# Kernel tuning notes

Hardware: AMD Instinct MI355X
Metric: run time of the kernel (lower is better)

## Reference

```python
import jax, jax.numpy as jnp
import numpy as np
from jax import lax

B, C, H, W = 8, 1, 256, 256
BIG = float(H + W)  # larger than any possible in-image distance


def _dist_1d_along_h(feat):
    # feat: bool (B,H,W). Exact 1D distance along axis 1 to nearest True pixel.
    def step(d, f):
        d = jnp.where(f, 0.0, d + 1.0)
        return d, d

    init = jnp.full((feat.shape[0], feat.shape[2]), BIG, dtype=jnp.float32)
    ft = jnp.moveaxis(feat, 1, 0)  # (H,B,W)
    _, fwd = lax.scan(step, init, ft)
    _, bwd = lax.scan(step, init, ft[::-1])
    g = jnp.minimum(fwd, bwd[::-1])  # (H,B,W)
    return jnp.moveaxis(g, 0, 1)  # (B,H,W)


def _edt(feat):
    # Exact 2D Euclidean distance transform to nearest True pixel.
    # Decomposition: D2(i,j) = min_{j'} ( g(i,j')^2 + (j-j')^2 ),
    # where g is the exact 1D vertical distance within each column.
    g = jnp.minimum(_dist_1d_along_h(feat), BIG)
    g2 = g * g  # (B,H,W')
    j = jnp.arange(feat.shape[2], dtype=jnp.float32)
    offs = (j[:, None] - j[None, :]) ** 2  # (W, W')
    d2 = jnp.min(g2[:, :, None, :] + offs[None, None, :, :], axis=-1)  # (B,H,W)
    return jnp.sqrt(d2)


def _level_set(targets):
    # Faithful port of compute_level_set_function.
    m = targets[:, 0] != 0  # (B,H,W) foreground
    # scipy.distance_transform_edt(mask): distance of nonzero pixels to nearest zero -> features = background
    dist_inside = _edt(~m)
    # distance_transform_edt(1-mask): features = foreground
    dist_outside = _edt(m)
    phi = dist_outside - dist_inside
    denom = jnp.max(jnp.abs(phi), axis=(1, 2), keepdims=True) + 1e-8
    phi = phi / denom
    has_fg = jnp.any(m, axis=(1, 2), keepdims=True)
    phi = jnp.where(has_fg, phi, 0.0)  # empty-mask short-circuit -> zeros
    return phi[:, None].astype(jnp.float32)  # (B,1,H,W)


def setup_inputs() -> dict:
    key = jax.random.key(0)
    k1, k2 = jax.random.split(key)
    predictions = jax.random.normal(k1, (B, C, H, W), dtype=jnp.float32)
    targets = jax.random.randint(k2, (B, C, H, W), 0, 2, dtype=jnp.int32)
    return {"predictions": predictions, "targets": targets}


def reference(predictions, targets):
    probs = jax.nn.sigmoid(predictions)
    phi_G = _level_set(targets)
    return jnp.mean(phi_G * probs)
```

## Files before the change

### kernel.cpp

```cpp
#include <hip/hip_runtime.h>
#include <math.h>

#define BB 8
#define HH 256
#define WW 256
#define NPIX (BB*HH*WW)
#define NROWS (BB*HH)


__global__ void colscan(const int* __restrict__ tgt,
                        float2* __restrict__ g2,
                        int* __restrict__ hasfg8) {
    __shared__ int hiF[8][32], loF[8][32], hiB[8][32], loB[8][32];
    __shared__ int wany[4];
    int tx = threadIdx.x;
    int c = tx & 31, s = tx >> 5;
    int bw = blockIdx.x;
    int b = bw >> 3;
    int w = ((bw & 7) << 5) + c;
    const int* col = tgt + b * HH * WW + w;
    int base = s << 5;

    unsigned fgbits = 0;
    #pragma unroll
    for (int r = 0; r < 32; ++r)
        fgbits |= (col[(base + r) * WW] != 0 ? 1u : 0u) << r;
    unsigned bgbits = ~fgbits;

    hiF[s][c] = fgbits ? (base + 31 - __clz(fgbits)) : -1;
    loF[s][c] = fgbits ? (base + __ffs(fgbits) - 1) : -1;
    hiB[s][c] = bgbits ? (base + 31 - __clz(bgbits)) : -1;
    loB[s][c] = bgbits ? (base + __ffs(bgbits) - 1) : -1;
    unsigned long long bal = __ballot(fgbits != 0);
    if ((tx & 63) == 0) wany[tx >> 6] = (bal != 0ull);
    __syncthreads();

    int prevF = -100000, nextF = 100000, prevB = -100000, nextB = 100000;
    for (int t = 0; t < s; ++t) {
        int h = hiF[t][c]; if (h >= 0) prevF = h;
        int g = hiB[t][c]; if (g >= 0) prevB = g;
    }
    for (int t = 7; t > s; --t) {
        int l = loF[t][c]; if (l >= 0) nextF = l;
        int m = loB[t][c]; if (m >= 0) nextB = m;
    }

    float2* out = g2 + b * HH * WW + w;
    #pragma unroll
    for (int r = 0; r < 32; ++r) {
        int i = base + r;
        unsigned lowmask = 0xFFFFFFFFu >> (31 - r);

        unsigned mf = fgbits & lowmask;
        int pF = mf ? (base + 31 - __clz(mf)) : prevF;
        unsigned nf = fgbits >> r;
        int nF = nf ? (i + __ffs(nf) - 1) : nextF;
        int gFg = min(min(i - pF, nF - i), 512);

        unsigned mb = bgbits & lowmask;
        int pB = mb ? (base + 31 - __clz(mb)) : prevB;
        unsigned nb = bgbits >> r;
        int nB = nb ? (i + __ffs(nb) - 1) : nextB;
        int gBg = min(min(i - pB, nB - i), 512);

        float fa = (float)gBg;
        float fb = (float)gFg;
        float2 o; o.x = fa * fa; o.y = fb * fb;
        out[i * WW] = o;
    }

    if (tx == 0)
        hasfg8[bw] = wany[0] | wany[1] | wany[2] | wany[3];
}

__global__ void edt_fuse(const float2* __restrict__ g2,
                         const float* __restrict__ pred,
                         float* __restrict__ part_max,
                         double* __restrict__ part_sum) {
    __shared__ float sB[3 * WW];
    __shared__ float sF[3 * WW];
    __shared__ float wmax[4];
    __shared__ double wsum[4];
    int row = blockIdx.x;
    int j = threadIdx.x;

    float x = pred[row * WW + j];
    float2 v = g2[row * WW + j];
    sB[j] = 1e30f; sB[2 * WW + j] = 1e30f; sB[WW + j] = v.x;
    sF[j] = 1e30f; sF[2 * WW + j] = 1e30f; sF[WW + j] = v.y;
    bool isBg = (v.x == 0.0f);
    __syncthreads();

    const float* sp = isBg ? sF : sB;
    float m = isBg ? v.y : v.x;
    int idx = WW + j;
    for (int k = 1; k < WW; ++k) {
        float k2 = (float)(k * k);
        if (k2 >= m) break;
        m = fminf(m, sp[idx - k] + k2);
        m = fminf(m, sp[idx + k] + k2);
    }
    float dist = sqrtf(m);
    float phi = isBg ? dist : -dist;
    float prob = 1.0f / (1.0f + expf(-x));
    double sd = (double)(phi * prob);
    float mx = dist;

    #pragma unroll
    for (int off = 32; off; off >>= 1) {
        mx = fmaxf(mx, __shfl_down(mx, off));
        sd += __shfl_down(sd, off);
    }
    int wid = j >> 6;
    if ((j & 63) == 0) { wmax[wid] = mx; wsum[wid] = sd; }
    __syncthreads();
    if (j == 0) {
        part_max[row] = fmaxf(fmaxf(wmax[0], wmax[1]), fmaxf(wmax[2], wmax[3]));
        part_sum[row] = wsum[0] + wsum[1] + wsum[2] + wsum[3];
    }
}

__global__ void reduce_out(const float* __restrict__ part_max,
                           const double* __restrict__ part_sum,
                           const int* __restrict__ hasfg8,
                           float* __restrict__ out) {
    __shared__ float wmax[4];
    __shared__ double wsum[4];
    int t = threadIdx.x;
    double total = 0.0;
    for (int b = 0; b < BB; ++b) {
        float mx = part_max[b * HH + t];
        double sd = part_sum[b * HH + t];
        #pragma unroll
        for (int off = 32; off; off >>= 1) {
            mx = fmaxf(mx, __shfl_down(mx, off));
            sd += __shfl_down(sd, off);
        }
        if ((t & 63) == 0) { wmax[t >> 6] = mx; wsum[t >> 6] = sd; }
        __syncthreads();
        if (t == 0) {
            int hf = 0;
            #pragma unroll
            for (int q = 0; q < 8; ++q) hf |= hasfg8[b * 8 + q];
            if (hf) {
                float mm = fmaxf(fmaxf(wmax[0], wmax[1]), fmaxf(wmax[2], wmax[3]));
                double dn = (double)mm + 1e-8;
                total += (wsum[0] + wsum[1] + wsum[2] + wsum[3]) / dn;
            }
        }
        __syncthreads();
    }
    if (t == 0) out[0] = (float)(total / (double)NPIX);
}

extern "C" void kernel_launch(void* const* d_in, const int* in_sizes, int n_in,
                              void* d_out, int out_size, void* d_ws, size_t ws_size,
                              hipStream_t stream) {
    const float* pred = (const float*)d_in[0];
    const int* tgt = (const int*)d_in[1];
    float* out = (float*)d_out;

    char* ws = (char*)d_ws;
    int* hasfg8 = (int*)ws;
    float* part_max = (float*)(ws + 4096);
    double* part_sum = (double*)(ws + 16384);
    float2* g2 = (float2*)(ws + 65536);

    colscan<<<64, 256, 0, stream>>>(tgt, g2, hasfg8);
    edt_fuse<<<NROWS, WW, 0, stream>>>(g2, pred, part_max, part_sum);
    reduce_out<<<1, 256, 0, stream>>>(part_max, part_sum, hasfg8, out);
}
```

Before: 70.93 us.

## Parallelize column scan with shuffle prefix scans and move fg detection to edt pass

```diff
diff --git a/kernel.cpp b/kernel.cpp
--- a/kernel.cpp
+++ b/kernel.cpp
@@ -9,78 +9,86 @@
 
 
 __global__ void colscan(const int* __restrict__ tgt,
-                        float2* __restrict__ g2,
-                        int* __restrict__ hasfg8) {
-    __shared__ int hiF[8][32], loF[8][32], hiB[8][32], loB[8][32];
-    __shared__ int wany[4];
+                        float2* __restrict__ g2) {
     int tx = threadIdx.x;
-    int c = tx & 31, s = tx >> 5;
+    int s = tx & 31, c = tx >> 5;
     int bw = blockIdx.x;
-    int b = bw >> 3;
-    int w = ((bw & 7) << 5) + c;
-    const int* col = tgt + b * HH * WW + w;
-    int base = s << 5;
+    int b = bw >> 4;
+    int w = ((bw & 15) << 4) + c;
+    const int* col = tgt + b * (HH * WW) + w;
+    int base = s << 3;
 
     unsigned fgbits = 0;
     #pragma unroll
-    for (int r = 0; r < 32; ++r)
+    for (int r = 0; r < 8; ++r)
         fgbits |= (col[(base + r) * WW] != 0 ? 1u : 0u) << r;
-    unsigned bgbits = ~fgbits;
+    unsigned bgbits = (~fgbits) & 0xFFu;
 
-    hiF[s][c] = fgbits ? (base + 31 - __clz(fgbits)) : -1;
-    loF[s][c] = fgbits ? (base + __ffs(fgbits) - 1) : -1;
-    hiB[s][c] = bgbits ? (base + 31 - __clz(bgbits)) : -1;
-    loB[s][c] = bgbits ? (base + __ffs(bgbits) - 1) : -1;
-    unsigned long long bal = __ballot(fgbits != 0);
-    if ((tx & 63) == 0) wany[tx >> 6] = (bal != 0ull);
-    __syncthreads();
+    const int BIGI = 1 << 20;
+    int hiF = fgbits ? base + (31 - __clz(fgbits)) : -1;
+    int hiB = bgbits ? base + (31 - __clz(bgbits)) : -1;
+    int loF = fgbits ? base + (__ffs(fgbits) - 1) : BIGI;
+    int loB = bgbits ? base + (__ffs(bgbits) - 1) : BIGI;
 
-    int prevF = -100000, nextF = 100000, prevB = -100000, nextB = 100000;
-    for (int t = 0; t < s; ++t) {
-        int h = hiF[t][c]; if (h >= 0) prevF = h;
-        int g = hiB[t][c]; if (g >= 0) prevB = g;
+    int aF = hiF, aB = hiB;
+    #pragma unroll
+    for (int d = 1; d < 32; d <<= 1) {
+        int vF = __shfl_up(aF, d, 32);
+        int vB = __shfl_up(aB, d, 32);
+        if (s >= d) { aF = max(aF, vF); aB = max(aB, vB); }
     }
-    for (int t = 7; t > s; --t) {
-        int l = loF[t][c]; if (l >= 0) nextF = l;
-        int m = loB[t][c]; if (m >= 0) nextB = m;
+    int pF = __shfl_up(aF, 1, 32);
+    int pB = __shfl_up(aB, 1, 32);
+    if (s == 0) { pF = -1; pB = -1; }
+    if (pF < 0) pF = -BIGI;
+    if (pB < 0) pB = -BIGI;
+
+    int cF = loF, cB = loB;
+    #pragma unroll
+    for (int d = 1; d < 32; d <<= 1) {
+        int vF = __shfl_down(cF, d, 32);
+        int vB = __shfl_down(cB, d, 32);
+        if (s < 32 - d) { cF = min(cF, vF); cB = min(cB, vB); }
+    }
+    int nF = __shfl_down(cF, 1, 32);
+    int nB = __shfl_down(cB, 1, 32);
+    if (s == 31) { nF = BIGI; nB = BIGI; }
+
+    int dDF[8], dDB[8];
+    int dF = nF - (base + 8);
+    int dB = nB - (base + 8);
+    #pragma unroll
+    for (int r = 7; r >= 0; --r) {
+        dF = ((fgbits >> r) & 1) ? 0 : dF + 1;
+        dB = ((bgbits >> r) & 1) ? 0 : dB + 1;
+        dDF[r] = dF; dDB[r] = dB;
     }
 
-    float2* out = g2 + b * HH * WW + w;
+    float2* out = g2 + b * (HH * WW) + w;
+    int uF = (base - 1) - pF;
+    int uB = (base - 1) - pB;
     #pragma unroll
-    for (int r = 0; r < 32; ++r) {
-        int i = base + r;
-        unsigned lowmask = 0xFFFFFFFFu >> (31 - r);
-
-        unsigned mf = fgbits & lowmask;
-        int pF = mf ? (base + 31 - __clz(mf)) : prevF;
-        unsigned nf = fgbits >> r;
-        int nF = nf ? (i + __ffs(nf) - 1) : nextF;
-        int gFg = min(min(i - pF, nF - i), 512);
-
-        unsigned mb = bgbits & lowmask;
-        int pB = mb ? (base + 31 - __clz(mb)) : prevB;
-        unsigned nb = bgbits >> r;
-        int nB = nb ? (i + __ffs(nb) - 1) : nextB;
-        int gBg = min(min(i - pB, nB - i), 512);
-
-        float fa = (float)gBg;
-        float fb = (float)gFg;
-        float2 o; o.x = fa * fa; o.y = fb * fb;
-        out[i * WW] = o;
+    for (int r = 0; r < 8; ++r) {
+        uF = ((fgbits >> r) & 1) ? 0 : uF + 1;
+        uB = ((bgbits >> r) & 1) ? 0 : uB + 1;
+        int gF = min(min(uF, dDF[r]), 512);
+        int gB = min(min(uB, dDB[r]), 512);
+        float fB = (float)gB, fF = (float)gF;
+        float2 o; o.x = fB * fB; o.y = fF * fF;
+        out[(base + r) * WW] = o;
     }
-
-    if (tx == 0)
-        hasfg8[bw] = wany[0] | wany[1] | wany[2] | wany[3];
 }
 
 __global__ void edt_fuse(const float2* __restrict__ g2,
                          const float* __restrict__ pred,
                          float* __restrict__ part_max,
-                         double* __restrict__ part_sum) {
+                         double* __restrict__ part_sum,
+                         int* __restrict__ part_fg) {
     __shared__ float sB[3 * WW];
     __shared__ float sF[3 * WW];
     __shared__ float wmax[4];
     __shared__ double wsum[4];
+    __shared__ int wfg[4];
     int row = blockIdx.x;
     int j = threadIdx.x;
 
@@ -89,6 +97,7 @@
     sB[j] = 1e30f; sB[2 * WW + j] = 1e30f; sB[WW + j] = v.x;
     sF[j] = 1e30f; sF[2 * WW + j] = 1e30f; sF[WW + j] = v.y;
     bool isBg = (v.x == 0.0f);
+    unsigned long long fgb = __ballot(v.y == 0.0f);
     __syncthreads();
 
     const float* sp = isBg ? sF : sB;
@@ -112,45 +121,47 @@
         sd += __shfl_down(sd, off);
     }
     int wid = j >> 6;
-    if ((j & 63) == 0) { wmax[wid] = mx; wsum[wid] = sd; }
+    if ((j & 63) == 0) { wmax[wid] = mx; wsum[wid] = sd; wfg[wid] = (fgb != 0ull); }
     __syncthreads();
     if (j == 0) {
         part_max[row] = fmaxf(fmaxf(wmax[0], wmax[1]), fmaxf(wmax[2], wmax[3]));
         part_sum[row] = wsum[0] + wsum[1] + wsum[2] + wsum[3];
+        part_fg[row] = wfg[0] | wfg[1] | wfg[2] | wfg[3];
     }
 }
 
 __global__ void reduce_out(const float* __restrict__ part_max,
                            const double* __restrict__ part_sum,
-                           const int* __restrict__ hasfg8,
+                           const int* __restrict__ part_fg,
                            float* __restrict__ out) {
-    __shared__ float wmax[4];
-    __shared__ double wsum[4];
-    int t = threadIdx.x;
-    double total = 0.0;
-    for (int b = 0; b < BB; ++b) {
-        float mx = part_max[b * HH + t];
-        double sd = part_sum[b * HH + t];
+    __shared__ double terms[8];
+    int tx = threadIdx.x;
+    int wv = tx >> 6, l = tx & 63;
+    #pragma unroll
+    for (int q = 0; q < 2; ++q) {
+        int b = wv * 2 + q;
+        int base = b * HH;
+        float mx = fmaxf(fmaxf(part_max[base + l], part_max[base + l + 64]),
+                         fmaxf(part_max[base + l + 128], part_max[base + l + 192]));
+        double sd = part_sum[base + l] + part_sum[base + l + 64]
+                  + part_sum[base + l + 128] + part_sum[base + l + 192];
+        int fg = part_fg[base + l] | part_fg[base + l + 64]
+               | part_fg[base + l + 128] | part_fg[base + l + 192];
         #pragma unroll
         for (int off = 32; off; off >>= 1) {
             mx = fmaxf(mx, __shfl_down(mx, off));
             sd += __shfl_down(sd, off);
+            fg |= __shfl_down(fg, off);
         }
-        if ((t & 63) == 0) { wmax[t >> 6] = mx; wsum[t >> 6] = sd; }
-        __syncthreads();
-        if (t == 0) {
-            int hf = 0;
-            #pragma unroll
-            for (int q = 0; q < 8; ++q) hf |= hasfg8[b * 8 + q];
-            if (hf) {
-                float mm = fmaxf(fmaxf(wmax[0], wmax[1]), fmaxf(wmax[2], wmax[3]));
-                double dn = (double)mm + 1e-8;
-                total += (wsum[0] + wsum[1] + wsum[2] + wsum[3]) / dn;
-            }
-        }
-        __syncthreads();
+        if (l == 0) terms[b] = fg ? sd / ((double)mx + 1e-8) : 0.0;
     }
-    if (t == 0) out[0] = (float)(total / (double)NPIX);
+    __syncthreads();
+    if (tx == 0) {
+        double t = 0.0;
+        #pragma unroll
+        for (int b = 0; b < BB; ++b) t += terms[b];
+        out[0] = (float)(t / (double)NPIX);
+    }
 }
 
 extern "C" void kernel_launch(void* const* d_in, const int* in_sizes, int n_in,
@@ -161,12 +172,12 @@
     float* out = (float*)d_out;
 
     char* ws = (char*)d_ws;
-    int* hasfg8 = (int*)ws;
-    float* part_max = (float*)(ws + 4096);
-    double* part_sum = (double*)(ws + 16384);
+    float* part_max = (float*)ws;
+    double* part_sum = (double*)(ws + 8192);
+    int* part_fg = (int*)(ws + 24576);
     float2* g2 = (float2*)(ws + 65536);
 
-    colscan<<<64, 256, 0, stream>>>(tgt, g2, hasfg8);
-    edt_fuse<<<NROWS, WW, 0, stream>>>(g2, pred, part_max, part_sum);
-    reduce_out<<<1, 256, 0, stream>>>(part_max, part_sum, hasfg8, out);
+    colscan<<<128, 512, 0, stream>>>(tgt, g2);
+    edt_fuse<<<NROWS, WW, 0, stream>>>(g2, pred, part_max, part_sum, part_fg);
+    reduce_out<<<1, 256, 0, stream>>>(part_max, part_sum, part_fg, out);
 }
```

New measurement: 67.15 us. -5.3%, faster.

## Fuse column scan and row EDT into one kernel using LDS column bitmasks

Applied to the files above, without the earlier changes.

```diff
diff --git a/kernel.cpp b/kernel.cpp
--- a/kernel.cpp
+++ b/kernel.cpp
@@ -5,152 +5,155 @@
 #define HH 256
 #define WW 256
 #define NPIX (BB*HH*WW)
-#define NROWS (BB*HH)
 
 
-__global__ void colscan(const int* __restrict__ tgt,
-                        float2* __restrict__ g2,
-                        int* __restrict__ hasfg8) {
-    __shared__ int hiF[8][32], loF[8][32], hiB[8][32], loB[8][32];
-    __shared__ int wany[4];
-    int tx = threadIdx.x;
-    int c = tx & 31, s = tx >> 5;
-    int bw = blockIdx.x;
-    int b = bw >> 3;
-    int w = ((bw & 7) << 5) + c;
-    const int* col = tgt + b * HH * WW + w;
-    int base = s << 5;
+__device__ __forceinline__ unsigned long long ldsW(const unsigned* fmL, int col, int w, bool inv) {
+    unsigned lo = fmL[col * 9 + 2 * w];
+    unsigned hi = fmL[col * 9 + 2 * w + 1];
+    unsigned long long v = ((unsigned long long)hi << 32) | lo;
+    return inv ? ~v : v;
+}
 
-    unsigned fgbits = 0;
+__device__ __forceinline__ int vdist_rest(const unsigned* fmL, int col, int wi, int bi,
+                                          unsigned long long cw, bool inv) {
+    unsigned long long up = cw & (~0ull >> (63 - bi));
+    unsigned long long dn = cw >> bi;
+    int du = 1 << 20, dd = 1 << 20;
+    if (up) du = bi - (63 - __builtin_clzll(up));
+    else {
+        for (int w = wi - 1; w >= 0; --w) {
+            unsigned long long v = ldsW(fmL, col, w, inv);
+            if (v) { du = bi + ((wi - w) << 6) - (63 - __builtin_clzll(v)); break; }
+        }
+    }
+    if (dn) dd = __builtin_ctzll(dn);
+    else {
+        for (int w = wi + 1; w < 4; ++w) {
+            unsigned long long v = ldsW(fmL, col, w, inv);
+            if (v) { dd = ((w - wi) << 6) - bi + __builtin_ctzll(v); break; }
+        }
+    }
+    return min(min(du, dd), 512);
+}
+
+__device__ __forceinline__ int vdistL(const unsigned* fmL, int col, int wi, int bi, bool inv) {
+    return vdist_rest(fmL, col, wi, bi, ldsW(fmL, col, wi, inv), inv);
+}
+
+__global__ void __launch_bounds__(1024)
+fused_edt(const int* __restrict__ tgt, const float* __restrict__ pred,
+          double* __restrict__ part_sum, float* __restrict__ part_max,
+          int* __restrict__ part_fg) {
+    __shared__ unsigned partLds[256 * 33];
+    __shared__ unsigned fmL[256 * 9];
+    __shared__ int wflag[16];
+    __shared__ float wmaxL[16];
+    __shared__ double wsumL[16];
+
+    int t = threadIdx.x;
+    int blk = blockIdx.x;
+    int batch = blk >> 3;
+    int i0 = (blk & 7) << 5;
+    int j = t & 255;
+    int q = t >> 8;
+
+    const int* tbase = tgt + batch * (HH * WW) + j;
     #pragma unroll
-    for (int r = 0; r < 32; ++r)
-        fgbits |= (col[(base + r) * WW] != 0 ? 1u : 0u) << r;
-    unsigned bgbits = ~fgbits;
-
-    hiF[s][c] = fgbits ? (base + 31 - __clz(fgbits)) : -1;
-    loF[s][c] = fgbits ? (base + __ffs(fgbits) - 1) : -1;
-    hiB[s][c] = bgbits ? (base + 31 - __clz(bgbits)) : -1;
-    loB[s][c] = bgbits ? (base + __ffs(bgbits) - 1) : -1;
-    unsigned long long bal = __ballot(fgbits != 0);
-    if ((tx & 63) == 0) wany[tx >> 6] = (bal != 0ull);
+    for (int w = 0; w < 8; ++w) {
+        unsigned pw = 0;
+        #pragma unroll
+        for (int m = 0; m < 8; ++m) {
+            int i = 32 * w + q + 4 * m;
+            pw |= (tbase[i * WW] != 0 ? 1u : 0u) << (q + 4 * m);
+        }
+        partLds[j * 33 + q * 8 + w] = pw;
+    }
     __syncthreads();
 
-    int prevF = -100000, nextF = 100000, prevB = -100000, nextB = 100000;
-    for (int t = 0; t < s; ++t) {
-        int h = hiF[t][c]; if (h >= 0) prevF = h;
-        int g = hiB[t][c]; if (g >= 0) prevB = g;
+    {
+        int jj = t >> 2, w2 = t & 3;
+        int pb = jj * 33;
+        unsigned lo = partLds[pb + 2 * w2]      | partLds[pb + 8 + 2 * w2]
+                    | partLds[pb + 16 + 2 * w2] | partLds[pb + 24 + 2 * w2];
+        unsigned hi = partLds[pb + 2 * w2 + 1]      | partLds[pb + 8 + 2 * w2 + 1]
+                    | partLds[pb + 16 + 2 * w2 + 1] | partLds[pb + 24 + 2 * w2 + 1];
+        fmL[jj * 9 + 2 * w2] = lo;
+        fmL[jj * 9 + 2 * w2 + 1] = hi;
+        unsigned long long bal = __ballot((lo | hi) != 0u);
+        if ((t & 63) == 0) wflag[t >> 6] = (bal != 0ull);
     }
-    for (int t = 7; t > s; --t) {
-        int l = loF[t][c]; if (l >= 0) nextF = l;
-        int m = loB[t][c]; if (m >= 0) nextB = m;
-    }
-
-    float2* out = g2 + b * HH * WW + w;
-    #pragma unroll
-    for (int r = 0; r < 32; ++r) {
-        int i = base + r;
-        unsigned lowmask = 0xFFFFFFFFu >> (31 - r);
-
-        unsigned mf = fgbits & lowmask;
-        int pF = mf ? (base + 31 - __clz(mf)) : prevF;
-        unsigned nf = fgbits >> r;
-        int nF = nf ? (i + __ffs(nf) - 1) : nextF;
-        int gFg = min(min(i - pF, nF - i), 512);
-
-        unsigned mb = bgbits & lowmask;
-        int pB = mb ? (base + 31 - __clz(mb)) : prevB;
-        unsigned nb = bgbits >> r;
-        int nB = nb ? (i + __ffs(nb) - 1) : nextB;
-        int gBg = min(min(i - pB, nB - i), 512);
-
-        float fa = (float)gBg;
-        float fb = (float)gFg;
-        float2 o; o.x = fa * fa; o.y = fb * fb;
-        out[i * WW] = o;
-    }
-
-    if (tx == 0)
-        hasfg8[bw] = wany[0] | wany[1] | wany[2] | wany[3];
-}
-
-__global__ void edt_fuse(const float2* __restrict__ g2,
-                         const float* __restrict__ pred,
-                         float* __restrict__ part_max,
-                         double* __restrict__ part_sum) {
-    __shared__ float sB[3 * WW];
-    __shared__ float sF[3 * WW];
-    __shared__ float wmax[4];
-    __shared__ double wsum[4];
-    int row = blockIdx.x;
-    int j = threadIdx.x;
-
-    float x = pred[row * WW + j];
-    float2 v = g2[row * WW + j];
-    sB[j] = 1e30f; sB[2 * WW + j] = 1e30f; sB[WW + j] = v.x;
-    sF[j] = 1e30f; sF[2 * WW + j] = 1e30f; sF[WW + j] = v.y;
-    bool isBg = (v.x == 0.0f);
     __syncthreads();
 
-    const float* sp = isBg ? sF : sB;
-    float m = isBg ? v.y : v.x;
-    int idx = WW + j;
-    for (int k = 1; k < WW; ++k) {
-        float k2 = (float)(k * k);
-        if (k2 >= m) break;
-        m = fminf(m, sp[idx - k] + k2);
-        m = fminf(m, sp[idx + k] + k2);
+    const float* pbase = pred + batch * (HH * WW);
+    double sd = 0.0;
+    float mx = 0.0f;
+    #pragma unroll
+    for (int it = 0; it < 8; ++it) {
+        int i = i0 + q + 4 * it;
+        float x = pbase[i * WW + j];
+        int wi = i >> 6, bi = i & 63;
+        unsigned long long w0 = ldsW(fmL, j, wi, false);
+        bool isFg = (w0 >> bi) & 1ull;
+        unsigned long long cw = isFg ? ~w0 : w0;
+        int d0 = vdist_rest(fmL, j, wi, bi, cw, isFg);
+        float m = (float)(d0 * d0);
+        for (int k = 1; k < WW; ++k) {
+            float k2 = (float)(k * k);
+            if (k2 >= m) break;
+            int jl = j - k; if (jl < 0) jl = 0;
+            int jr = j + k; if (jr > 255) jr = 255;
+            int dl = vdistL(fmL, jl, wi, bi, isFg);
+            m = fminf(m, (float)(dl * dl) + k2);
+            int dr = vdistL(fmL, jr, wi, bi, isFg);
+            m = fminf(m, (float)(dr * dr) + k2);
+        }
+        float dist = sqrtf(m);
+        float phi = isFg ? -dist : dist;
+        float prob = 1.0f / (1.0f + expf(-x));
+        sd += (double)(phi * prob);
+        mx = fmaxf(mx, dist);
     }
-    float dist = sqrtf(m);
-    float phi = isBg ? dist : -dist;
-    float prob = 1.0f / (1.0f + expf(-x));
-    double sd = (double)(phi * prob);
-    float mx = dist;
 
     #pragma unroll
     for (int off = 32; off; off >>= 1) {
         mx = fmaxf(mx, __shfl_down(mx, off));
         sd += __shfl_down(sd, off);
     }
-    int wid = j >> 6;
-    if ((j & 63) == 0) { wmax[wid] = mx; wsum[wid] = sd; }
+    if ((t & 63) == 0) { wmaxL[t >> 6] = mx; wsumL[t >> 6] = sd; }
     __syncthreads();
-    if (j == 0) {
-        part_max[row] = fmaxf(fmaxf(wmax[0], wmax[1]), fmaxf(wmax[2], wmax[3]));
-        part_sum[row] = wsum[0] + wsum[1] + wsum[2] + wsum[3];
+    if (t == 0) {
+        float M = 0.0f; double S = 0.0; int F = 0;
+        #pragma unroll
+        for (int wv = 0; wv < 16; ++wv) {
+            M = fmaxf(M, wmaxL[wv]); S += wsumL[wv]; F |= wflag[wv];
+        }
+        part_max[blk] = M; part_sum[blk] = S; part_fg[blk] = F;
     }
 }
 
-__global__ void reduce_out(const float* __restrict__ part_max,
-                           const double* __restrict__ part_sum,
-                           const int* __restrict__ hasfg8,
+__global__ void reduce_out(const double* __restrict__ part_sum,
+                           const float* __restrict__ part_max,
+                           const int* __restrict__ part_fg,
                            float* __restrict__ out) {
-    __shared__ float wmax[4];
-    __shared__ double wsum[4];
+    __shared__ double terms[8];
     int t = threadIdx.x;
-    double total = 0.0;
-    for (int b = 0; b < BB; ++b) {
-        float mx = part_max[b * HH + t];
-        double sd = part_sum[b * HH + t];
+    double sd = part_sum[t];
+    float mx = part_max[t];
+    int fg = part_fg[t];
+    #pragma unroll
+    for (int off = 4; off; off >>= 1) {
+        sd += __shfl_down(sd, off);
+        mx = fmaxf(mx, __shfl_down(mx, off));
+        fg |= __shfl_down(fg, off);
+    }
+    if ((t & 7) == 0) terms[t >> 3] = fg ? sd / ((double)mx + 1e-8) : 0.0;
+    __syncthreads();
+    if (t == 0) {
+        double tot = 0.0;
         #pragma unroll
-        for (int off = 32; off; off >>= 1) {
-            mx = fmaxf(mx, __shfl_down(mx, off));
-            sd += __shfl_down(sd, off);
-        }
-        if ((t & 63) == 0) { wmax[t >> 6] = mx; wsum[t >> 6] = sd; }
-        __syncthreads();
-        if (t == 0) {
-            int hf = 0;
-            #pragma unroll
-            for (int q = 0; q < 8; ++q) hf |= hasfg8[b * 8 + q];
-            if (hf) {
-                float mm = fmaxf(fmaxf(wmax[0], wmax[1]), fmaxf(wmax[2], wmax[3]));
-                double dn = (double)mm + 1e-8;
-                total += (wsum[0] + wsum[1] + wsum[2] + wsum[3]) / dn;
-            }
-        }
-        __syncthreads();
+        for (int b = 0; b < BB; ++b) tot += terms[b];
+        out[0] = (float)(tot / (double)NPIX);
     }
-    if (t == 0) out[0] = (float)(total / (double)NPIX);
 }
 
 extern "C" void kernel_launch(void* const* d_in, const int* in_sizes, int n_in,
@@ -161,12 +164,10 @@
     float* out = (float*)d_out;
 
     char* ws = (char*)d_ws;
-    int* hasfg8 = (int*)ws;
-    float* part_max = (float*)(ws + 4096);
-    double* part_sum = (double*)(ws + 16384);
-    float2* g2 = (float2*)(ws + 65536);
+    double* part_sum = (double*)ws;
+    float* part_max = (float*)(ws + 1024);
+    int* part_fg = (int*)(ws + 2048);
 
-    colscan<<<64, 256, 0, stream>>>(tgt, g2, hasfg8);
-    edt_fuse<<<NROWS, WW, 0, stream>>>(g2, pred, part_max, part_sum);
-    reduce_out<<<1, 256, 0, stream>>>(part_max, part_sum, hasfg8, out);
+    fused_edt<<<64, 1024, 0, stream>>>(tgt, pred, part_sum, part_max, part_fg);
+    reduce_out<<<1, 64, 0, stream>>>(part_sum, part_max, part_fg, out);
 }
```

New measurement: 72.62 us. +2.4%, slower.
